# Optimization experiments

Measured on AMD Instinct MI355X. Metric: run time of the kernel, lower is better.

Reference implementation:

```python
import jax, jax.numpy as jnp
import numpy as np

D_MODEL = 1024
NUM_HEADS = 16
D_HEAD = D_MODEL // NUM_HEADS


def setup_inputs() -> dict:
    key = jax.random.key(0)
    ks = jax.random.split(key, 9)
    s = 1.0 / np.sqrt(D_MODEL)
    x = jax.random.normal(ks[0], (2, 2048, D_MODEL), dtype=jnp.float32)
    wq = jax.random.normal(ks[1], (D_MODEL, D_MODEL), dtype=jnp.float32) * s
    wk = jax.random.normal(ks[2], (D_MODEL, D_MODEL), dtype=jnp.float32) * s
    wv = jax.random.normal(ks[3], (D_MODEL, D_MODEL), dtype=jnp.float32) * s
    wo = jax.random.normal(ks[4], (D_MODEL, D_MODEL), dtype=jnp.float32) * s
    bq = jax.random.normal(ks[5], (D_MODEL,), dtype=jnp.float32) * s
    bk = jax.random.normal(ks[6], (D_MODEL,), dtype=jnp.float32) * s
    bv = jax.random.normal(ks[7], (D_MODEL,), dtype=jnp.float32) * s
    bo = jax.random.normal(ks[8], (D_MODEL,), dtype=jnp.float32) * s
    return {"x": x, "wq": wq, "bq": bq, "wk": wk, "bk": bk,
            "wv": wv, "bv": bv, "wo": wo, "bo": bo}


def _split_heads(t):
    b, s, _ = t.shape
    return t.reshape(b, s, NUM_HEADS, D_HEAD).transpose(0, 2, 1, 3)  # [b,h,s,dh]


def reference(x, wq, bq, wk, bk, wv, bv, wo, bo):
    b, s, d = x.shape
    q = _split_heads(x @ wq + bq)
    k = _split_heads(x @ wk + bk)
    v = _split_heads(x @ wv + bv)
    scale = 1.0 / jnp.sqrt(jnp.asarray(D_HEAD, x.dtype))
    scores = jnp.einsum('bhqd,bhkd->bhqk', q, k) * scale  # [b,h,s,s]
    weights = jax.nn.softmax(scores, axis=-1)
    attended = jnp.einsum('bhqk,bhkd->bhqd', weights, v)
    attended = attended.transpose(0, 2, 1, 3).reshape(b, s, d)
    out = attended @ wo + bo
    return out, weights
```

## Files before the change

kernel.cpp:

```cpp
#include <hip/hip_runtime.h>
#include <math.h>


typedef unsigned short u16;
typedef __attribute__((ext_vector_type(8))) short bf16x8;
typedef __attribute__((ext_vector_type(4))) float f32x4;

__device__ __forceinline__ u16 f2bf(float f) {
  union { float f; unsigned u; } v;
  v.f = f;
  unsigned r = v.u + 0x7fffu + ((v.u >> 16) & 1u);
  return (u16)(r >> 16);
}

#define GLD16(g, l)                                       \
  __builtin_amdgcn_global_load_lds(                       \
      (const __attribute__((address_space(1))) void*)(g), \
      (__attribute__((address_space(3))) void*)(l), 16, 0, 0)

template <int ROWS>
__device__ __forceinline__ void stage_bf16(const u16* __restrict__ src, int ld,
                                           u16* dst, int wid, int lane) {
  constexpr int NCH = ROWS / 16;
#pragma unroll
  for (int c = wid; c < NCH; c += 4) {
    const u16* g = src + (size_t)(c * 16 + (lane >> 2)) * ld + (lane & 3) * 8;
    u16* l = dst + c * 512 + lane * 8;
    GLD16(g, l);
  }
}

template <int BM, int BN, int WM, int WN, bool AF32, bool OBF16>
__global__ __launch_bounds__(256) void mm_nt(
    const void* __restrict__ A, const u16* __restrict__ B,
    const float* __restrict__ bias, void* __restrict__ C, int K, int lda,
    int ldb, int ldc, size_t sAb, size_t sAh, size_t sBb, size_t sBh,
    size_t sCb, size_t sCh, int hdiv, float alpha) {
  constexpr int WAVES_N = BN / WN;
  constexpr int MR = WM / 16, NR = WN / 16;
  static_assert((BM / WM) * (BN / WN) == 4, "4 waves");
  __shared__ u16 As[BM * 32];
  __shared__ u16 Bs[BN * 32];

  const int z = blockIdx.z;
  const int bb = z / hdiv, hh = z % hdiv;
  const int row0 = blockIdx.y * BM;
  const int col0 = blockIdx.x * BN;
  const int tid = threadIdx.x;
  const int lane = tid & 63, wid = tid >> 6;
  const int wm0 = (wid / WAVES_N) * WM;
  const int wn0 = (wid % WAVES_N) * WN;
  const int lw = lane & 15, lg = lane >> 4;

  const float* Afb = nullptr;
  const u16* Aub = nullptr;
  if constexpr (AF32)
    Afb = (const float*)A + (size_t)bb * sAb + (size_t)hh * sAh +
          (size_t)row0 * lda;
  else
    Aub = (const u16*)A + (size_t)bb * sAb + (size_t)hh * sAh +
          (size_t)row0 * lda;
  const u16* Bsrc =
      B + (size_t)bb * sBb + (size_t)hh * sBh + (size_t)col0 * ldb;

  f32x4 acc[MR][NR] = {};

  for (int k0 = 0; k0 < K; k0 += 32) {
    if constexpr (AF32) {
#pragma unroll
      for (int p = 0; p < BM / 32; ++p) {
        const int e = (p * 256 + tid) * 4;
        const int r = e >> 5, k = e & 31;
        const float4 v = *(const float4*)(Afb + (size_t)r * lda + (k0 + k));
        *(ushort4*)&As[r * 32 + k] =
            make_ushort4(f2bf(v.x), f2bf(v.y), f2bf(v.z), f2bf(v.w));
      }
    } else {
      stage_bf16<BM>(Aub + k0, lda, As, wid, lane);
    }
    stage_bf16<BN>(Bsrc + k0, ldb, Bs, wid, lane);
    __syncthreads();

    bf16x8 af[MR], bfr[NR];
#pragma unroll
    for (int mi = 0; mi < MR; ++mi)
      af[mi] = *(const bf16x8*)&As[(wm0 + mi * 16 + lw) * 32 + lg * 8];
#pragma unroll
    for (int nj = 0; nj < NR; ++nj)
      bfr[nj] = *(const bf16x8*)&Bs[(wn0 + nj * 16 + lw) * 32 + lg * 8];
#pragma unroll
    for (int mi = 0; mi < MR; ++mi)
#pragma unroll
      for (int nj = 0; nj < NR; ++nj)
        acc[mi][nj] = __builtin_amdgcn_mfma_f32_16x16x32_bf16(
            af[mi], bfr[nj], acc[mi][nj], 0, 0, 0);
    __syncthreads();
  }

  float* Cf = nullptr;
  u16* Cu = nullptr;
  if constexpr (OBF16)
    Cu = (u16*)C + (size_t)bb * sCb + (size_t)hh * sCh;
  else
    Cf = (float*)C + (size_t)bb * sCb + (size_t)hh * sCh;
#pragma unroll
  for (int mi = 0; mi < MR; ++mi) {
#pragma unroll
    for (int nj = 0; nj < NR; ++nj) {
      const int c = col0 + wn0 + nj * 16 + lw;
      const float bv = bias ? bias[c] : 0.f;
#pragma unroll
      for (int q = 0; q < 4; ++q) {
        const int r = row0 + wm0 + mi * 16 + lg * 4 + q;
        const float v = alpha * acc[mi][nj][q] + bv;
        if constexpr (OBF16)
          Cu[(size_t)r * ldc + c] = f2bf(v);
        else
          Cf[(size_t)r * ldc + c] = v;
      }
    }
  }
}

__global__ __launch_bounds__(256) void cvt_x_kernel(
    const float* __restrict__ src, u16* __restrict__ dst, int n4) {
  int i = blockIdx.x * 256 + threadIdx.x;
  const int stride = gridDim.x * 256;
  for (; i < n4; i += stride) {
    const float4 v = ((const float4*)src)[i];
    ((ushort4*)dst)[i] = make_ushort4(f2bf(v.x), f2bf(v.y), f2bf(v.z), f2bf(v.w));
  }
}

__global__ __launch_bounds__(256) void wtrans_kernel(
    const float* __restrict__ src, u16* __restrict__ dst) {
  __shared__ float t[32][33];
  const int tx = threadIdx.x % 32, ty = threadIdx.x / 32;
  const int r0 = blockIdx.y * 32, c0 = blockIdx.x * 32;
#pragma unroll
  for (int i = 0; i < 32; i += 8)
    t[ty + i][tx] = src[(size_t)(r0 + ty + i) * 1024 + c0 + tx];
  __syncthreads();
#pragma unroll
  for (int i = 0; i < 32; i += 8)
    dst[(size_t)(c0 + ty + i) * 1024 + r0 + tx] = f2bf(t[tx][ty + i]);
}

__global__ __launch_bounds__(256) void vtrans_kernel(
    const u16* __restrict__ src, u16* __restrict__ dst) {
  __shared__ u16 t[32][33];
  const size_t zo = (size_t)blockIdx.z * 2048 * 1024;
  const int tx = threadIdx.x % 32, ty = threadIdx.x / 32;
  const int r0 = blockIdx.y * 32, c0 = blockIdx.x * 32;
#pragma unroll
  for (int i = 0; i < 32; i += 8)
    t[ty + i][tx] = src[zo + (size_t)(r0 + ty + i) * 1024 + c0 + tx];
  __syncthreads();
#pragma unroll
  for (int i = 0; i < 32; i += 8)
    dst[zo + (size_t)(c0 + ty + i) * 2048 + r0 + tx] = t[tx][ty + i];
}

__global__ __launch_bounds__(256) void softmax_kernel(float* __restrict__ w) {
  const size_t row = blockIdx.x;
  float* p = w + row * 2048;
  const int tid = threadIdx.x;
  const int wave = tid >> 6, lane = tid & 63;

  float v[8];
  float m = -1e30f;
#pragma unroll
  for (int i = 0; i < 8; i++) {
    v[i] = p[tid + i * 256];
    m = fmaxf(m, v[i]);
  }
#pragma unroll
  for (int off = 32; off > 0; off >>= 1) m = fmaxf(m, __shfl_xor(m, off, 64));
  __shared__ float redm[4];
  if (lane == 0) redm[wave] = m;
  __syncthreads();
  m = fmaxf(fmaxf(redm[0], redm[1]), fmaxf(redm[2], redm[3]));

  float s = 0.f;
#pragma unroll
  for (int i = 0; i < 8; i++) {
    v[i] = __expf(v[i] - m);
    s += v[i];
  }
#pragma unroll
  for (int off = 32; off > 0; off >>= 1) s += __shfl_xor(s, off, 64);
  __shared__ float reds[4];
  if (lane == 0) reds[wave] = s;
  __syncthreads();
  s = reds[0] + reds[1] + reds[2] + reds[3];

  const float inv = 1.0f / s;
#pragma unroll
  for (int i = 0; i < 8; i++) p[tid + i * 256] = v[i] * inv;
}

extern "C" void kernel_launch(void* const* d_in, const int* in_sizes, int n_in,
                              void* d_out, int out_size, void* d_ws,
                              size_t ws_size, hipStream_t stream) {
  const float* x = (const float*)d_in[0];
  const float* wq = (const float*)d_in[1];
  const float* bq = (const float*)d_in[2];
  const float* wk = (const float*)d_in[3];
  const float* bk = (const float*)d_in[4];
  const float* wv = (const float*)d_in[5];
  const float* bv = (const float*)d_in[6];
  const float* wo = (const float*)d_in[7];
  const float* bo = (const float*)d_in[8];

  const int Bz = 2, S = 2048, D = 1024, H = 16;
  const size_t MS = (size_t)Bz * S;

  float* out = (float*)d_out;
  float* wts = out + MS * D;

  u16* xb = (u16*)d_ws;
  u16* wqt = xb + MS * D;
  u16* wkt = wqt + (size_t)D * D;
  u16* wvt = wkt + (size_t)D * D;
  u16* wot = wvt + (size_t)D * D;
  u16* Qb = wot + (size_t)D * D;
  u16* Kb = Qb + MS * D;
  u16* Vb = Kb + MS * D;
  u16* Vt = Vb + MS * D;
  u16* Attb = Vt + MS * D;

  dim3 blk(256);

  cvt_x_kernel<<<1024, blk, 0, stream>>>(x, xb, (int)(MS * D / 4));
  wtrans_kernel<<<dim3(32, 32), blk, 0, stream>>>(wq, wqt);
  wtrans_kernel<<<dim3(32, 32), blk, 0, stream>>>(wk, wkt);
  wtrans_kernel<<<dim3(32, 32), blk, 0, stream>>>(wv, wvt);
  wtrans_kernel<<<dim3(32, 32), blk, 0, stream>>>(wo, wot);

  dim3 gproj(D / 128, (int)(MS / 64), 1);
  mm_nt<64, 128, 32, 64, false, true><<<gproj, blk, 0, stream>>>(
      xb, wqt, bq, Qb, D, D, D, D, 0, 0, 0, 0, 0, 0, 1, 1.f);
  mm_nt<64, 128, 32, 64, false, true><<<gproj, blk, 0, stream>>>(
      xb, wkt, bk, Kb, D, D, D, D, 0, 0, 0, 0, 0, 0, 1, 1.f);
  mm_nt<64, 128, 32, 64, false, true><<<gproj, blk, 0, stream>>>(
      xb, wvt, bv, Vb, D, D, D, D, 0, 0, 0, 0, 0, 0, 1, 1.f);

  vtrans_kernel<<<dim3(32, 64, 2), blk, 0, stream>>>(Vb, Vt);

  dim3 gsc(S / 128, S / 128, Bz * H);
  mm_nt<128, 128, 64, 64, false, false><<<gsc, blk, 0, stream>>>(
      Qb, Kb, nullptr, wts, 64, D, D, S, (size_t)S * D, 64, (size_t)S * D, 64,
      (size_t)H * S * S, (size_t)S * S, H, 0.125f);

  softmax_kernel<<<(int)(Bz * H * S), blk, 0, stream>>>(wts);

  dim3 gav(1, S / 64, Bz * H);
  mm_nt<64, 64, 32, 32, true, true><<<gav, blk, 0, stream>>>(
      wts, Vt, nullptr, Attb, S, S, S, D, (size_t)H * S * S, (size_t)S * S,
      (size_t)D * S, (size_t)64 * S, (size_t)S * D, 64, H, 1.f);

  mm_nt<64, 128, 32, 64, false, false><<<gproj, blk, 0, stream>>>(
      Attb, wot, bo, out, D, D, D, D, 0, 0, 0, 0, 0, 0, 1, 1.f);
}
```

Baseline: 1.093 ms.

## Fuse QK^T scoring with softmax, merge QKV projections, and write bf16 probabilities

Adds a 1024-thread kernel in which each block computes a 32-row slice of full 2048-wide score rows. It keeps those scores in registers, performs softmax there, and writes the fp32 weights once, which removes the separate scores write plus softmax read/write pass. The three Q/K/V projections are merged into one GEMM with a packed weight and bias, writing a [MS, 3D] interleaved buffer. When workspace allows, a bf16 copy of the probabilities is also written so the AV GEMM can stage it with global_load_lds instead of converting fp32 on the fly. The cost is an extra 256MB-scale bf16 write, plus a large-block kernel with limited occupancy and heavy register use.

Result: faster. 919.7 us (-15.8%).

```diff
diff --git a/kernel.cpp b/kernel.cpp
--- a/kernel.cpp
+++ b/kernel.cpp
@@ -18,12 +18,12 @@
       (const __attribute__((address_space(1))) void*)(g), \
       (__attribute__((address_space(3))) void*)(l), 16, 0, 0)
 
-template <int ROWS>
-__device__ __forceinline__ void stage_bf16(const u16* __restrict__ src, int ld,
-                                           u16* dst, int wid, int lane) {
+template <int ROWS, int NW>
+__device__ __forceinline__ void stage_g(const u16* __restrict__ src, int ld,
+                                        u16* dst, int wid, int lane) {
   constexpr int NCH = ROWS / 16;
 #pragma unroll
-  for (int c = wid; c < NCH; c += 4) {
+  for (int c = wid; c < NCH; c += NW) {
     const u16* g = src + (size_t)(c * 16 + (lane >> 2)) * ld + (lane & 3) * 8;
     u16* l = dst + c * 512 + lane * 8;
     GLD16(g, l);
@@ -76,9 +76,9 @@
             make_ushort4(f2bf(v.x), f2bf(v.y), f2bf(v.z), f2bf(v.w));
       }
     } else {
-      stage_bf16<BM>(Aub + k0, lda, As, wid, lane);
-    }
-    stage_bf16<BN>(Bsrc + k0, ldb, Bs, wid, lane);
+      stage_g<BM, 4>((const u16*)Aub + k0, lda, As, wid, lane);
+    }
+    stage_g<BN, 4>(Bsrc + k0, ldb, Bs, wid, lane);
     __syncthreads();
 
     bf16x8 af[MR], bfr[NR];
@@ -122,14 +122,161 @@
   }
 }
 
+template <bool WRITE_P>
+__global__ __launch_bounds__(1024) void score_softmax_kernel(
+    const u16* __restrict__ QKV, float* __restrict__ W, u16* __restrict__ P) {
+  __shared__ u16 Ks[512 * 32];
+  __shared__ u16 Qs[2][32 * 32];
+  __shared__ float red[2][32][16];
+
+  const int bid = blockIdx.x;
+  const int swz = (bid & 7) * 256 + (bid >> 3);
+  const int z = swz >> 6;
+  const int rb = swz & 63;
+  const int bb = z >> 4, hh = z & 15;
+  const int row0 = rb * 32;
+
+  const int tid = threadIdx.x;
+  const int lane = tid & 63, wid = tid >> 6;
+  const int lw = lane & 15, lg = lane >> 4;
+
+  const u16* Qh = QKV + (size_t)bb * 2048 * 3072 + (size_t)hh * 64;
+  const u16* Kh = Qh + 1024;
+
+  f32x4 acc[2][8] = {};
+  bf16x8 af[2][2];
+
+#pragma unroll
+  for (int ph = 0; ph < 8; ++ph) {
+    const int qr = ph >> 1, kc2 = ph & 1;
+    stage_g<512, 16>(Kh + (size_t)(qr * 512) * 3072 + kc2 * 32, 3072, Ks, wid,
+                     lane);
+    if (ph == 0) {
+      stage_g<32, 16>(Qh + (size_t)row0 * 3072, 3072, Qs[0], wid, lane);
+      stage_g<32, 16>(Qh + (size_t)row0 * 3072 + 32, 3072, Qs[1], wid, lane);
+    }
+    __syncthreads();
+    if (ph == 0) {
+#pragma unroll
+      for (int kc = 0; kc < 2; ++kc)
+#pragma unroll
+        for (int mi = 0; mi < 2; ++mi)
+          af[mi][kc] = *(const bf16x8*)&Qs[kc][(mi * 16 + lw) * 32 + lg * 8];
+    }
+#pragma unroll
+    for (int nj = 0; nj < 2; ++nj) {
+      const bf16x8 bf =
+          *(const bf16x8*)&Ks[(wid * 32 + nj * 16 + lw) * 32 + lg * 8];
+#pragma unroll
+      for (int mi = 0; mi < 2; ++mi)
+        acc[mi][qr * 2 + nj] = __builtin_amdgcn_mfma_f32_16x16x32_bf16(
+            af[mi][kc2], bf, acc[mi][qr * 2 + nj], 0, 0, 0);
+    }
+    if (ph < 7) __syncthreads();
+  }
+
+  float rm[2][4], rs[2][4];
+#pragma unroll
+  for (int mi = 0; mi < 2; ++mi)
+#pragma unroll
+    for (int q = 0; q < 4; ++q) {
+      float m = -1e30f;
+#pragma unroll
+      for (int a = 0; a < 8; ++a) {
+        acc[mi][a][q] *= 0.125f;
+        m = fmaxf(m, acc[mi][a][q]);
+      }
+#pragma unroll
+      for (int off = 8; off >= 1; off >>= 1)
+        m = fmaxf(m, __shfl_xor(m, off, 64));
+      rm[mi][q] = m;
+    }
+  if (lw == 0) {
+#pragma unroll
+    for (int mi = 0; mi < 2; ++mi)
+#pragma unroll
+      for (int q = 0; q < 4; ++q)
+        red[0][mi * 16 + lg * 4 + q][wid] = rm[mi][q];
+  }
+  __syncthreads();
+#pragma unroll
+  for (int mi = 0; mi < 2; ++mi)
+#pragma unroll
+    for (int q = 0; q < 4; ++q) {
+      float m = -1e30f;
+#pragma unroll
+      for (int w = 0; w < 16; ++w)
+        m = fmaxf(m, red[0][mi * 16 + lg * 4 + q][w]);
+      rm[mi][q] = m;
+    }
+
+#pragma unroll
+  for (int mi = 0; mi < 2; ++mi)
+#pragma unroll
+    for (int q = 0; q < 4; ++q) {
+      float s = 0.f;
+#pragma unroll
+      for (int a = 0; a < 8; ++a) {
+        const float e = __expf(acc[mi][a][q] - rm[mi][q]);
+        acc[mi][a][q] = e;
+        s += e;
+      }
+#pragma unroll
+      for (int off = 8; off >= 1; off >>= 1) s += __shfl_xor(s, off, 64);
+      rs[mi][q] = s;
+    }
+  if (lw == 0) {
+#pragma unroll
+    for (int mi = 0; mi < 2; ++mi)
+#pragma unroll
+      for (int q = 0; q < 4; ++q)
+        red[1][mi * 16 + lg * 4 + q][wid] = rs[mi][q];
+  }
+  __syncthreads();
+#pragma unroll
+  for (int mi = 0; mi < 2; ++mi)
+#pragma unroll
+    for (int q = 0; q < 4; ++q) {
+      float s = 0.f;
+#pragma unroll
+      for (int w = 0; w < 16; ++w) s += red[1][mi * 16 + lg * 4 + q][w];
+      rs[mi][q] = 1.0f / s;
+    }
+
+  float* Wh = W + ((size_t)(bb * 16 + hh) * 2048 + row0) * 2048;
+  u16* Ph = P + ((size_t)(bb * 16 + hh) * 2048 + row0) * 2048;
+#pragma unroll
+  for (int mi = 0; mi < 2; ++mi)
+#pragma unroll
+    for (int q = 0; q < 4; ++q) {
+      const int r = mi * 16 + lg * 4 + q;
+      const float inv = rs[mi][q];
+#pragma unroll
+      for (int a = 0; a < 8; ++a) {
+        const int c = (a >> 1) * 512 + wid * 32 + (a & 1) * 16 + lw;
+        const float v = acc[mi][a][q] * inv;
+        Wh[(size_t)r * 2048 + c] = v;
+        if constexpr (WRITE_P) Ph[(size_t)r * 2048 + c] = f2bf(v);
+      }
+    }
+}
+
 __global__ __launch_bounds__(256) void cvt_x_kernel(
     const float* __restrict__ src, u16* __restrict__ dst, int n4) {
   int i = blockIdx.x * 256 + threadIdx.x;
   const int stride = gridDim.x * 256;
   for (; i < n4; i += stride) {
     const float4 v = ((const float4*)src)[i];
-    ((ushort4*)dst)[i] = make_ushort4(f2bf(v.x), f2bf(v.y), f2bf(v.z), f2bf(v.w));
-  }
+    ((ushort4*)dst)[i] =
+        make_ushort4(f2bf(v.x), f2bf(v.y), f2bf(v.z), f2bf(v.w));
+  }
+}
+
+__global__ __launch_bounds__(1024) void pack_bias_kernel(
+    const float* __restrict__ bq, const float* __restrict__ bk,
+    const float* __restrict__ bv, float* __restrict__ dst) {
+  const float* src = blockIdx.x == 0 ? bq : (blockIdx.x == 1 ? bk : bv);
+  dst[blockIdx.x * 1024 + threadIdx.x] = src[threadIdx.x];
 }
 
 __global__ __launch_bounds__(256) void wtrans_kernel(
@@ -147,56 +294,19 @@
 }
 
 __global__ __launch_bounds__(256) void vtrans_kernel(
-    const u16* __restrict__ src, u16* __restrict__ dst) {
+    const u16* __restrict__ src, u16* __restrict__ dst, int ld) {
   __shared__ u16 t[32][33];
-  const size_t zo = (size_t)blockIdx.z * 2048 * 1024;
   const int tx = threadIdx.x % 32, ty = threadIdx.x / 32;
   const int r0 = blockIdx.y * 32, c0 = blockIdx.x * 32;
+  const size_t so = (size_t)blockIdx.z * 2048 * ld;
+  const size_t dz = (size_t)blockIdx.z * 1024 * 2048;
 #pragma unroll
   for (int i = 0; i < 32; i += 8)
-    t[ty + i][tx] = src[zo + (size_t)(r0 + ty + i) * 1024 + c0 + tx];
+    t[ty + i][tx] = src[so + (size_t)(r0 + ty + i) * ld + c0 + tx];
   __syncthreads();
 #pragma unroll
   for (int i = 0; i < 32; i += 8)
-    dst[zo + (size_t)(c0 + ty + i) * 2048 + r0 + tx] = t[tx][ty + i];
-}
-
-__global__ __launch_bounds__(256) void softmax_kernel(float* __restrict__ w) {
-  const size_t row = blockIdx.x;
-  float* p = w + row * 2048;
-  const int tid = threadIdx.x;
-  const int wave = tid >> 6, lane = tid & 63;
-
-  float v[8];
-  float m = -1e30f;
-#pragma unroll
-  for (int i = 0; i < 8; i++) {
-    v[i] = p[tid + i * 256];
-    m = fmaxf(m, v[i]);
-  }
-#pragma unroll
-  for (int off = 32; off > 0; off >>= 1) m = fmaxf(m, __shfl_xor(m, off, 64));
-  __shared__ float redm[4];
-  if (lane == 0) redm[wave] = m;
-  __syncthreads();
-  m = fmaxf(fmaxf(redm[0], redm[1]), fmaxf(redm[2], redm[3]));
-
-  float s = 0.f;
-#pragma unroll
-  for (int i = 0; i < 8; i++) {
-    v[i] = __expf(v[i] - m);
-    s += v[i];
-  }
-#pragma unroll
-  for (int off = 32; off > 0; off >>= 1) s += __shfl_xor(s, off, 64);
-  __shared__ float reds[4];
-  if (lane == 0) reds[wave] = s;
-  __syncthreads();
-  s = reds[0] + reds[1] + reds[2] + reds[3];
-
-  const float inv = 1.0f / s;
-#pragma unroll
-  for (int i = 0; i < 8; i++) p[tid + i * 256] = v[i] * inv;
+    dst[dz + (size_t)(c0 + ty + i) * 2048 + r0 + tx] = t[tx][ty + i];
 }
 
 extern "C" void kernel_launch(void* const* d_in, const int* in_sizes, int n_in,
@@ -219,46 +329,48 @@
   float* wts = out + MS * D;
 
   u16* xb = (u16*)d_ws;
-  u16* wqt = xb + MS * D;
-  u16* wkt = wqt + (size_t)D * D;
-  u16* wvt = wkt + (size_t)D * D;
-  u16* wot = wvt + (size_t)D * D;
-  u16* Qb = wot + (size_t)D * D;
-  u16* Kb = Qb + MS * D;
-  u16* Vb = Kb + MS * D;
-  u16* Vt = Vb + MS * D;
-  u16* Attb = Vt + MS * D;
+  u16* wall = xb + MS * D;
+  u16* qkv = wall + (size_t)4 * D * D;
+  u16* Vt = qkv + MS * 3 * D;
+  u16* Attb = Vt + (size_t)Bz * D * S;
+  float* bqkv = (float*)(Attb + MS * D);
+  u16* Pb = (u16*)(bqkv + 3 * D);
+  const size_t need_p =
+      (size_t)((char*)Pb - (char*)d_ws) + MS * (size_t)H * S * 2 * 2;
+  const bool use_p = ws_size >= need_p;
 
   dim3 blk(256);
 
   cvt_x_kernel<<<1024, blk, 0, stream>>>(x, xb, (int)(MS * D / 4));
-  wtrans_kernel<<<dim3(32, 32), blk, 0, stream>>>(wq, wqt);
-  wtrans_kernel<<<dim3(32, 32), blk, 0, stream>>>(wk, wkt);
-  wtrans_kernel<<<dim3(32, 32), blk, 0, stream>>>(wv, wvt);
-  wtrans_kernel<<<dim3(32, 32), blk, 0, stream>>>(wo, wot);
-
-  dim3 gproj(D / 128, (int)(MS / 64), 1);
+  wtrans_kernel<<<dim3(32, 32), blk, 0, stream>>>(wq, wall);
+  wtrans_kernel<<<dim3(32, 32), blk, 0, stream>>>(wk, wall + (size_t)D * D);
+  wtrans_kernel<<<dim3(32, 32), blk, 0, stream>>>(wv, wall + (size_t)2 * D * D);
+  wtrans_kernel<<<dim3(32, 32), blk, 0, stream>>>(wo, wall + (size_t)3 * D * D);
+  pack_bias_kernel<<<3, dim3(1024), 0, stream>>>(bq, bk, bv, bqkv);
+
+  dim3 gproj(3 * D / 128, (int)(MS / 64), 1);
   mm_nt<64, 128, 32, 64, false, true><<<gproj, blk, 0, stream>>>(
-      xb, wqt, bq, Qb, D, D, D, D, 0, 0, 0, 0, 0, 0, 1, 1.f);
-  mm_nt<64, 128, 32, 64, false, true><<<gproj, blk, 0, stream>>>(
-      xb, wkt, bk, Kb, D, D, D, D, 0, 0, 0, 0, 0, 0, 1, 1.f);
-  mm_nt<64, 128, 32, 64, false, true><<<gproj, blk, 0, stream>>>(
-      xb, wvt, bv, Vb, D, D, D, D, 0, 0, 0, 0, 0, 0, 1, 1.f);
-
-  vtrans_kernel<<<dim3(32, 64, 2), blk, 0, stream>>>(Vb, Vt);
-
-  dim3 gsc(S / 128, S / 128, Bz * H);
-  mm_nt<128, 128, 64, 64, false, false><<<gsc, blk, 0, stream>>>(
-      Qb, Kb, nullptr, wts, 64, D, D, S, (size_t)S * D, 64, (size_t)S * D, 64,
-      (size_t)H * S * S, (size_t)S * S, H, 0.125f);
-
-  softmax_kernel<<<(int)(Bz * H * S), blk, 0, stream>>>(wts);
+      xb, wall, bqkv, qkv, D, D, D, 3 * D, 0, 0, 0, 0, 0, 0, 1, 1.f);
+
+  vtrans_kernel<<<dim3(32, 64, 2), blk, 0, stream>>>(qkv + 2 * D, Vt, 3 * D);
+
+  if (use_p)
+    score_softmax_kernel<true><<<2048, dim3(1024), 0, stream>>>(qkv, wts, Pb);
+  else
+    score_softmax_kernel<false><<<2048, dim3(1024), 0, stream>>>(qkv, wts, Pb);
 
   dim3 gav(1, S / 64, Bz * H);
-  mm_nt<64, 64, 32, 32, true, true><<<gav, blk, 0, stream>>>(
-      wts, Vt, nullptr, Attb, S, S, S, D, (size_t)H * S * S, (size_t)S * S,
-      (size_t)D * S, (size_t)64 * S, (size_t)S * D, 64, H, 1.f);
-
-  mm_nt<64, 128, 32, 64, false, false><<<gproj, blk, 0, stream>>>(
-      Attb, wot, bo, out, D, D, D, D, 0, 0, 0, 0, 0, 0, 1, 1.f);
-}
+  if (use_p)
+    mm_nt<64, 64, 32, 32, false, true><<<gav, blk, 0, stream>>>(
+        Pb, Vt, nullptr, Attb, S, S, S, D, (size_t)H * S * S, (size_t)S * S,
+        (size_t)D * S, (size_t)64 * S, (size_t)S * D, 64, H, 1.f);
+  else
+    mm_nt<64, 64, 32, 32, true, true><<<gav, blk, 0, stream>>>(
+        wts, Vt, nullptr, Attb, S, S, S, D, (size_t)H * S * S, (size_t)S * S,
+        (size_t)D * S, (size_t)64 * S, (size_t)S * D, 64, H, 1.f);
+
+  dim3 gout(D / 128, (int)(MS / 64), 1);
+  mm_nt<64, 128, 32, 64, false, false><<<gout, blk, 0, stream>>>(
+      Attb, wall + (size_t)3 * D * D, bo, out, D, D, D, D, 0, 0, 0, 0, 0, 0, 1,
+      1.f);
+}
```
